# Kernel optimization log

Hardware: AMD Instinct MI355X
Metric: run time of the kernel (lower is better)

## Reference

```python
import jax, jax.numpy as jnp
import numpy as np

N_HIDDEN = 512
N_MEMORY = 128
BUDGET = 16
BATCH = 32768


def setup_inputs() -> dict:
    key = jax.random.key(0)
    ks = jax.random.split(key, 4)
    s1 = 1.0 / np.sqrt(N_HIDDEN + N_MEMORY)
    s2 = 1.0 / np.sqrt(2048)
    return {
        "x": jax.random.normal(ks[0], (BATCH, N_HIDDEN), dtype=jnp.float32),
        "W1": jax.random.normal(ks[1], (N_HIDDEN + N_MEMORY, 2048), dtype=jnp.float32) * s1,
        "b1": jnp.zeros((2048,), dtype=jnp.float32),
        "W2": jax.random.normal(ks[2], (2048, 2048), dtype=jnp.float32) * s2,
        "b2": jnp.zeros((2048,), dtype=jnp.float32),
        "W3": jax.random.normal(ks[3], (2048, N_HIDDEN + N_MEMORY + 2), dtype=jnp.float32) * s2,
        "b3": jnp.zeros((N_HIDDEN + N_MEMORY + 2,), dtype=jnp.float32),
    }


def reference(x, W1, b1, W2, b2, W3, b3):
    batch = x.shape[0]
    dtype = x.dtype

    memory = jnp.zeros((batch, N_MEMORY), dtype=dtype).at[:, 0].set(float(BUDGET))
    halted = jnp.zeros((batch,), dtype=bool)
    final_probs = jnp.zeros((batch,), dtype=dtype)
    n_iters = jnp.zeros((batch,), dtype=dtype)  # never updated in the original forward

    def mlp(inp):
        h = jax.nn.relu(inp @ W1 + b1)
        h = jax.nn.relu(h @ W2 + b2)
        return h @ W3 + b3

    def step(carry, _):
        x, mem, halted, fp = carry
        out = mlp(jnp.concatenate([x, mem], axis=-1))  # [B, 2+H+M]
        probs = out[:, 0]
        halt_val = out[:, 1]
        hidden_out = out[:, 2:2 + N_HIDDEN]
        mem_out = out[:, 2 + N_HIDDEN:]
        active = ~halted
        # torch compacts with boolean masks; masked-where is the dense equivalent
        x = jnp.where(active[:, None], hidden_out, x)
        mem = jnp.where(active[:, None], mem_out, mem)
        halt = jax.nn.sigmoid(halt_val) > 0.5  # sigmoid().round().bool()
        newly = active & halt
        fp = jnp.where(newly, probs, fp)
        halted = halted | newly
        return (x, mem, halted, fp), None

    (x, memory, halted, final_probs), _ = jax.lax.scan(
        step, (x, memory, halted, final_probs), None, length=BUDGET)

    return jax.nn.sigmoid(final_probs), n_iters
```

## Files before the change

kernel.cpp:

```cpp
#include <hip/hip_runtime.h>
#include <math.h>

typedef _Float16 f16;
typedef _Float16 f16x8 __attribute__((ext_vector_type(8)));
typedef float f32x4 __attribute__((ext_vector_type(4)));

#define NB 32768
#define NH 512
#define NM 128
#define NIN 640
#define NHID 2048
#define NOUT 642
#define NOUTP 768
#define ITERS 16
#define S1 2048.0f
#define EPS1 4.8828125e-4f

__device__ __forceinline__ void gload16(const void* g, void* lds) {
  __builtin_amdgcn_global_load_lds(
      reinterpret_cast<const __attribute__((address_space(1))) unsigned int*>((uintptr_t)g),
      reinterpret_cast<__attribute__((address_space(3))) unsigned int*>((unsigned int)(uintptr_t)lds),
      16, 0, 0);
}

__device__ __forceinline__ f32x4 mfma16(f16x8 a, f16x8 b, f32x4 c) {
  return __builtin_amdgcn_mfma_f32_16x16x32_f16(a, b, c, 0, 0, 0);
}

__device__ __forceinline__ void split2(float v, f16& a0, f16& a1) {
  a0 = (f16)v;
  a1 = (f16)((v - (float)a0) * S1);
}

__global__ void k_prepW(const float* __restrict__ W, f16* __restrict__ WT,
                        int K, int Nreal) {
  __shared__ float tile[32][33];
  int k0 = blockIdx.x * 32, n0 = blockIdx.y * 32;
  int tx = threadIdx.x & 31, ty = threadIdx.x >> 5;
#pragma unroll
  for (int r = 0; r < 4; ++r) {
    int kk = ty + 8 * r;
    int n = n0 + tx;
    tile[kk][tx] = (n < Nreal) ? W[(size_t)(k0 + kk) * Nreal + n] : 0.0f;
  }
  __syncthreads();
#pragma unroll
  for (int r = 0; r < 4; ++r) {
    int nl = ty + 8 * r;
    float v = tile[tx][nl];
    f16 a0, a1; split2(v, a0, a1);
    size_t o = (size_t)(n0 + nl) * (2 * K) + k0 + tx;
    WT[o] = a0; WT[o + K] = a1;
  }
}

__global__ void k_splitX(const float* __restrict__ x, f16* __restrict__ xm2) {
  int i = blockIdx.x * 256 + threadIdx.x;
  int row = i >> 9, c = i & 511;
  f16 a0, a1; split2(x[i], a0, a1);
  size_t o = (size_t)row * (2 * NIN) + c;
  xm2[o] = a0; xm2[o + NIN] = a1;
}

__global__ void k_init(f16* __restrict__ xm2, float* __restrict__ fpb,
                       int* __restrict__ list0, int* __restrict__ cnt) {
  int gid = blockIdx.x * blockDim.x + threadIdx.x;
  if (gid < NB * NM) {
    int row = gid >> 7, c = gid & 127;
    size_t o = (size_t)row * (2 * NIN) + 512 + c;
    xm2[o] = (f16)((c == 0) ? 16.0f : 0.0f);
    xm2[o + NIN] = (f16)0.0f;
  }
  if (gid < NB) { fpb[gid] = 0.0f; list0[gid] = gid; }
  if (gid < 32) cnt[gid] = (gid == 0) ? NB : 0;
}


#define GEMM_PREAMBLE()                                                     \
  int tid = threadIdx.x;                                                    \
  int w = tid >> 6, lane = tid & 63;                                        \
  int lm = lane & 15, kb = lane >> 4;                                       \
  int kidx = ((kb ^ ((lm >> 1) & 3)) << 3);                                 \
  int ksrc = (((tid & 3) ^ ((tid >> 3) & 3)) << 3);                         \
  int stg = tid * 8;                                                        \
  int afo[4], bfo[2];                                                       \
  _Pragma("unroll") for (int m = 0; m < 4; ++m)                             \
    afo[m] = (m * 16 + lm) * 32 + kidx;                                     \
  _Pragma("unroll") for (int n = 0; n < 2; ++n)                             \
    bfo[n] = (w * 32 + n * 16 + lm) * 32 + kidx + 4096;                     \
  f32x4 acc0[4][2], acc1[4][2];                                             \
  _Pragma("unroll") for (int m = 0; m < 4; ++m)                             \
  _Pragma("unroll") for (int n = 0; n < 2; ++n) {                           \
    acc0[m][n] = (f32x4)0.0f; acc1[m][n] = (f32x4)0.0f;                     \
  }

#define GEMM_COMPUTE(BASE)                                                  \
  {                                                                         \
    const f16* _sb = (BASE);                                                \
    f16x8 fa0[4], fa1[4], fb0[2], fb1[2];                                   \
    _Pragma("unroll") for (int m = 0; m < 4; ++m) {                         \
      fa0[m] = *(const f16x8*)&_sb[afo[m]];                                 \
      fa1[m] = *(const f16x8*)&_sb[2048 + afo[m]];                          \
    }                                                                       \
    _Pragma("unroll") for (int n = 0; n < 2; ++n) {                         \
      fb0[n] = *(const f16x8*)&_sb[bfo[n]];                                 \
      fb1[n] = *(const f16x8*)&_sb[4096 + bfo[n]];                          \
    }                                                                       \
    __builtin_amdgcn_s_setprio(1);                                          \
    _Pragma("unroll") for (int m = 0; m < 4; ++m)                           \
    _Pragma("unroll") for (int n = 0; n < 2; ++n) {                         \
      acc0[m][n] = mfma16(fa0[m], fb0[n], acc0[m][n]);                      \
      acc1[m][n] = mfma16(fa0[m], fb1[n], acc1[m][n]);                      \
      acc1[m][n] = mfma16(fa1[m], fb0[n], acc1[m][n]);                      \
    }                                                                       \
    __builtin_amdgcn_s_setprio(0);                                          \
  }

#define STAGE6(K0, DST, PSA, PSB)                                           \
  {                                                                         \
    _Pragma("unroll") for (int s = 0; s < 2; ++s)                           \
      gload16(pA + s * (PSA) + (K0), (DST) + s * 2048 + stg);               \
    _Pragma("unroll") for (int s = 0; s < 2; ++s) {                         \
      gload16(pB + s * (PSB) + (K0), (DST) + 4096 + s * 4096 + stg);        \
      gload16(pB2 + s * (PSB) + (K0), (DST) + 6144 + s * 4096 + stg);       \
    }                                                                       \
  }

#define GEMM_PIPELOOP(KTOT, PSA, PSB)                                       \
  STAGE6(0, &SB[0], PSA, PSB);                                              \
  __syncthreads();                                                          \
  {                                                                         \
    int pb = 0;                                                             \
    for (int k0 = 0; k0 < (KTOT); k0 += 32, pb ^= 1) {                      \
      if (k0 + 32 < (KTOT))                                                 \
        STAGE6(k0 + 32, pb ? &SB[0] : &SB[12288], PSA, PSB);                \
      GEMM_COMPUTE(pb ? &SB[12288] : &SB[0]);                               \
      __syncthreads();                                                      \
    }                                                                       \
  }

#define COMBINE(m, n, q) (acc0[m][n][q] + EPS1 * acc1[m][n][q])

#define MAP16(ID, BX, NY) int NY = ((ID) & 7) + 8 * (((ID) >> 3) & 1); int BX = (ID) >> 4;

__global__ __launch_bounds__(256) void k_l1(
    const f16* __restrict__ xm2, const f16* __restrict__ WT,
    const float* __restrict__ b1, f16* __restrict__ h1,
    const int* __restrict__ list, const int* __restrict__ cntp,
    int chunk_off, int chunk_rows) {
  int cnt = *cntp;
  MAP16(blockIdx.x, bx, ny);
  int lm0 = bx * 64;
  if (chunk_off + lm0 >= cnt) return;
  int lim = cnt - chunk_off; if (lim > chunk_rows) lim = chunk_rows;
  int n0 = ny * 128;

  __shared__ f16 SB[2 * 12288];
  GEMM_PREAMBLE();

  int pu = chunk_off + lm0 + (tid >> 2);
  int idx = list[pu < cnt ? pu : (cnt - 1)];
  const f16* pA = xm2 + (size_t)idx * (2 * NIN) + ksrc;
  const f16* pB = WT + (size_t)(n0 + (tid >> 2)) * (2 * NIN) + ksrc;
  const f16* pB2 = pB + (size_t)64 * (2 * NIN);

  GEMM_PIPELOOP(NIN, NIN, NIN);

#pragma unroll
  for (int n = 0; n < 2; ++n) {
    int col = n0 + w * 32 + n * 16 + lm;
    float bb = b1[col];
#pragma unroll
    for (int m = 0; m < 4; ++m) {
#pragma unroll
      for (int q = 0; q < 4; ++q) {
        int gr = lm0 + m * 16 + kb * 4 + q;
        if (gr < lim) {
          float v = fmaxf(COMBINE(m, n, q) + bb, 0.0f);
          f16 a0, a1; split2(v, a0, a1);
          size_t o = (size_t)gr * (2 * NHID) + col;
          h1[o] = a0; h1[o + NHID] = a1;
        }
      }
    }
  }
}

__global__ __launch_bounds__(256) void k_l2(
    const f16* __restrict__ h1, const f16* __restrict__ WT,
    const float* __restrict__ b2, f16* __restrict__ h2,
    const int* __restrict__ cntp, int chunk_off, int chunk_rows) {
  int cnt = *cntp;
  MAP16(blockIdx.x, bx, ny);
  int lm0 = bx * 64;
  if (chunk_off + lm0 >= cnt) return;
  int lim = cnt - chunk_off; if (lim > chunk_rows) lim = chunk_rows;
  int n0 = ny * 128;

  __shared__ f16 SB[2 * 12288];
  GEMM_PREAMBLE();

  const f16* pA = h1 + (size_t)(lm0 + (tid >> 2)) * (2 * NHID) + ksrc;
  const f16* pB = WT + (size_t)(n0 + (tid >> 2)) * (2 * NHID) + ksrc;
  const f16* pB2 = pB + (size_t)64 * (2 * NHID);

  GEMM_PIPELOOP(NHID, NHID, NHID);

#pragma unroll
  for (int n = 0; n < 2; ++n) {
    int col = n0 + w * 32 + n * 16 + lm;
    float bb = b2[col];
#pragma unroll
    for (int m = 0; m < 4; ++m) {
#pragma unroll
      for (int q = 0; q < 4; ++q) {
        int gr = lm0 + m * 16 + kb * 4 + q;
        if (gr < lim) {
          float v = fmaxf(COMBINE(m, n, q) + bb, 0.0f);
          f16 a0, a1; split2(v, a0, a1);
          size_t o = (size_t)gr * (2 * NHID) + col;
          h2[o] = a0; h2[o + NHID] = a1;
        }
      }
    }
  }
}

__global__ __launch_bounds__(256) void k_l3(
    const f16* __restrict__ h2, const f16* __restrict__ WT,
    const float* __restrict__ b3, f16* __restrict__ xm2,
    float* __restrict__ probs, float* __restrict__ hv,
    const int* __restrict__ list, const int* __restrict__ cntp,
    int chunk_off, int chunk_rows) {
  int cnt = *cntp;
  int id = blockIdx.x;
  int bx = id / 6, ny = id - bx * 6;
  int lm0 = bx * 64;
  if (chunk_off + lm0 >= cnt) return;
  int lim = cnt - chunk_off; if (lim > chunk_rows) lim = chunk_rows;
  int n0 = ny * 128;

  __shared__ f16 SB[2 * 12288];
  GEMM_PREAMBLE();

  const f16* pA = h2 + (size_t)(lm0 + (tid >> 2)) * (2 * NHID) + ksrc;
  const f16* pB = WT + (size_t)(n0 + (tid >> 2)) * (2 * NHID) + ksrc;
  const f16* pB2 = pB + (size_t)64 * (2 * NHID);

  GEMM_PIPELOOP(NHID, NHID, NHID);

  float bb[2]; int colv[2];
#pragma unroll
  for (int n = 0; n < 2; ++n) {
    colv[n] = n0 + w * 32 + n * 16 + lm;
    bb[n] = (colv[n] < NOUT) ? b3[colv[n]] : 0.0f;
  }
#pragma unroll
  for (int m = 0; m < 4; ++m) {
#pragma unroll
    for (int q = 0; q < 4; ++q) {
      int gr = lm0 + m * 16 + kb * 4 + q;
      if (gr >= lim) continue;
      int r = list[chunk_off + gr];
#pragma unroll
      for (int n = 0; n < 2; ++n) {
        int col = colv[n];
        if (col >= NOUT) continue;
        float v = COMBINE(m, n, q) + bb[n];
        if (col == 0) {
          probs[r] = v;
        } else if (col == 1) {
          hv[r] = v;
        } else if (col < 2 + NH) {
          f16 a0, a1; split2(v, a0, a1);
          size_t o = (size_t)r * (2 * NIN) + (col - 2);
          xm2[o] = a0; xm2[o + NIN] = a1;
        } else {
          f16 a0, a1; split2(v, a0, a1);
          size_t o = (size_t)r * (2 * NIN) + 512 + (col - 2 - NH);
          xm2[o] = a0; xm2[o + NIN] = a1;
        }
      }
    }
  }
}

__global__ void k_update(const int* __restrict__ listc, int* __restrict__ listn,
                         const float* __restrict__ hv, const float* __restrict__ probs,
                         float* __restrict__ fpb, const int* __restrict__ cntc,
                         int* __restrict__ cntn) {
  int i = blockIdx.x * blockDim.x + threadIdx.x;
  if (i >= *cntc) return;
  int r = listc[i];
  if (hv[r] > 0.0f) {
    fpb[r] = probs[r];
  } else {
    int pos = atomicAdd(cntn, 1);
    listn[pos] = r;
  }
}

__global__ void k_final(const float* __restrict__ fpb, float* __restrict__ out) {
  int i = blockIdx.x * blockDim.x + threadIdx.x;
  if (i < NB) {
    out[i] = 1.0f / (1.0f + expf(-fpb[i]));
    out[NB + i] = 0.0f;
  }
}

extern "C" void kernel_launch(void* const* d_in, const int* in_sizes, int n_in,
                              void* d_out, int out_size, void* d_ws, size_t ws_size,
                              hipStream_t stream) {
  const float* x  = (const float*)d_in[0];
  const float* W1 = (const float*)d_in[1];
  const float* b1 = (const float*)d_in[2];
  const float* W2 = (const float*)d_in[3];
  const float* b2 = (const float*)d_in[4];
  const float* W3 = (const float*)d_in[5];
  const float* b3 = (const float*)d_in[6];
  float* out = (float*)d_out;

  char* p = (char*)d_ws;
  auto alloc = [&](size_t bytes) {
    char* r = p;
    p += (bytes + 255) & ~(size_t)255;
    return r;
  };
  f16* xm2  = (f16*)alloc((size_t)NB * 2 * NIN * 2);
  f16* W1T  = (f16*)alloc((size_t)NHID * 2 * NIN * 2);
  f16* W2T  = (f16*)alloc((size_t)NHID * 2 * NHID * 2);
  f16* W3T  = (f16*)alloc((size_t)NOUTP * 2 * NHID * 2);
  float* probs = (float*)alloc((size_t)NB * 4);
  float* hvb   = (float*)alloc((size_t)NB * 4);
  float* fpb   = (float*)alloc((size_t)NB * 4);
  int* list0   = (int*)alloc((size_t)NB * 4);
  int* list1   = (int*)alloc((size_t)NB * 4);
  int* cnt     = (int*)alloc(32 * 4);

  size_t used = (size_t)(p - (char*)d_ws);
  size_t remain = (ws_size > used) ? (ws_size - used) : 0;
  long long chl = (long long)(remain / ((size_t)2 * 2 * NHID * 2));
  int CH = (int)(chl > NB ? NB : chl);
  CH &= ~127;
  if (CH < 128) CH = 128;
  f16* h1 = (f16*)alloc((size_t)CH * 2 * NHID * 2);
  f16* h2 = (f16*)alloc((size_t)CH * 2 * NHID * 2);
  int nchunks = (NB + CH - 1) / CH;

  k_prepW<<<dim3(NIN / 32, NHID / 32), 256, 0, stream>>>(W1, W1T, NIN, NHID);
  k_prepW<<<dim3(NHID / 32, NHID / 32), 256, 0, stream>>>(W2, W2T, NHID, NHID);
  k_prepW<<<dim3(NHID / 32, NOUTP / 32), 256, 0, stream>>>(W3, W3T, NHID, NOUT);
  k_splitX<<<(NB * NH) / 256, 256, 0, stream>>>(x, xm2);
  k_init<<<(NB * NM) / 256, 256, 0, stream>>>(xm2, fpb, list0, cnt);

  for (int t = 0; t < ITERS; ++t) {
    const int* lc = (t & 1) ? list1 : list0;
    int* ln       = (t & 1) ? list0 : list1;
    const int* cc = cnt + t;
    int* cn       = cnt + t + 1;
    for (int c = 0; c < nchunks; ++c) {
      int off = c * CH;
      int rows = NB - off; if (rows > CH) rows = CH;
      int g1 = (CH / 64) * 16;
      k_l1<<<g1, 256, 0, stream>>>(xm2, W1T, b1, h1, lc, cc, off, rows);
      k_l2<<<g1, 256, 0, stream>>>(h1, W2T, b2, h2, cc, off, rows);
      int g3 = (CH / 64) * 6;
      k_l3<<<g3, 256, 0, stream>>>(h2, W3T, b3, xm2, probs, hvb, lc, cc, off, rows);
    }
    k_update<<<NB / 256, 256, 0, stream>>>(lc, ln, hvb, probs, fpb, cc, cn);
  }
  k_final<<<NB / 256, 256, 0, stream>>>(fpb, out);
}
```

Before: 4.392 ms.

## Enlarge GEMM block tile to 128x128 with 2x2 wave layout

Each GEMM block now covers 128 rows by 128 columns instead of 64x128. The four waves are arranged 2x2, each computing a 64x64 subtile with 4x4 MFMA accumulators. The goal is more reuse of each LDS fragment per MFMA and less global and LDS traffic per flop. In exchange, registers double (acc0/acc1 now 4x4) and LDS per block grows to 64KB, with launch_bounds(256,2) added to keep two blocks per CU. Grids are halved, and tail chunks with few active rows waste more work per block.

```diff
diff --git a/kernel.cpp b/kernel.cpp
--- a/kernel.cpp
+++ b/kernel.cpp
@@ -79,36 +79,37 @@
 #define GEMM_PREAMBLE()                                                     \
   int tid = threadIdx.x;                                                    \
   int w = tid >> 6, lane = tid & 63;                                        \
+  int wr = w >> 1, wc = w & 1;                                              \
   int lm = lane & 15, kb = lane >> 4;                                       \
   int kidx = ((kb ^ ((lm >> 1) & 3)) << 3);                                 \
   int ksrc = (((tid & 3) ^ ((tid >> 3) & 3)) << 3);                         \
   int stg = tid * 8;                                                        \
-  int afo[4], bfo[2];                                                       \
+  int afo[4], bfo[4];                                                       \
   _Pragma("unroll") for (int m = 0; m < 4; ++m)                             \
-    afo[m] = (m * 16 + lm) * 32 + kidx;                                     \
-  _Pragma("unroll") for (int n = 0; n < 2; ++n)                             \
-    bfo[n] = (w * 32 + n * 16 + lm) * 32 + kidx + 4096;                     \
-  f32x4 acc0[4][2], acc1[4][2];                                             \
+    afo[m] = (wr * 64 + m * 16 + lm) * 32 + kidx;                           \
+  _Pragma("unroll") for (int n = 0; n < 4; ++n)                             \
+    bfo[n] = (wc * 64 + n * 16 + lm) * 32 + kidx + 8192;                    \
+  f32x4 acc0[4][4], acc1[4][4];                                             \
   _Pragma("unroll") for (int m = 0; m < 4; ++m)                             \
-  _Pragma("unroll") for (int n = 0; n < 2; ++n) {                           \
+  _Pragma("unroll") for (int n = 0; n < 4; ++n) {                           \
     acc0[m][n] = (f32x4)0.0f; acc1[m][n] = (f32x4)0.0f;                     \
   }
 
 #define GEMM_COMPUTE(BASE)                                                  \
   {                                                                         \
     const f16* _sb = (BASE);                                                \
-    f16x8 fa0[4], fa1[4], fb0[2], fb1[2];                                   \
+    f16x8 fa0[4], fa1[4], fb0[4], fb1[4];                                   \
     _Pragma("unroll") for (int m = 0; m < 4; ++m) {                         \
       fa0[m] = *(const f16x8*)&_sb[afo[m]];                                 \
-      fa1[m] = *(const f16x8*)&_sb[2048 + afo[m]];                          \
-    }                                                                       \
-    _Pragma("unroll") for (int n = 0; n < 2; ++n) {                         \
+      fa1[m] = *(const f16x8*)&_sb[4096 + afo[m]];                          \
+    }                                                                       \
+    _Pragma("unroll") for (int n = 0; n < 4; ++n) {                         \
       fb0[n] = *(const f16x8*)&_sb[bfo[n]];                                 \
       fb1[n] = *(const f16x8*)&_sb[4096 + bfo[n]];                          \
     }                                                                       \
     __builtin_amdgcn_s_setprio(1);                                          \
     _Pragma("unroll") for (int m = 0; m < 4; ++m)                           \
-    _Pragma("unroll") for (int n = 0; n < 2; ++n) {                         \
+    _Pragma("unroll") for (int n = 0; n < 4; ++n) {                         \
       acc0[m][n] = mfma16(fa0[m], fb0[n], acc0[m][n]);                      \
       acc1[m][n] = mfma16(fa0[m], fb1[n], acc1[m][n]);                      \
       acc1[m][n] = mfma16(fa1[m], fb0[n], acc1[m][n]);                      \
@@ -116,25 +117,27 @@
     __builtin_amdgcn_s_setprio(0);                                          \
   }
 
-#define STAGE6(K0, DST, PSA, PSB)                                           \
+#define STAGE8(K0, DST, PSA, PSB)                                           \
   {                                                                         \
-    _Pragma("unroll") for (int s = 0; s < 2; ++s)                           \
-      gload16(pA + s * (PSA) + (K0), (DST) + s * 2048 + stg);               \
     _Pragma("unroll") for (int s = 0; s < 2; ++s) {                         \
-      gload16(pB + s * (PSB) + (K0), (DST) + 4096 + s * 4096 + stg);        \
-      gload16(pB2 + s * (PSB) + (K0), (DST) + 6144 + s * 4096 + stg);       \
+      gload16(pA + s * (PSA) + (K0), (DST) + s * 4096 + stg);               \
+      gload16(pA2 + s * (PSA) + (K0), (DST) + 2048 + s * 4096 + stg);       \
+    }                                                                       \
+    _Pragma("unroll") for (int s = 0; s < 2; ++s) {                         \
+      gload16(pB + s * (PSB) + (K0), (DST) + 8192 + s * 4096 + stg);        \
+      gload16(pB2 + s * (PSB) + (K0), (DST) + 10240 + s * 4096 + stg);      \
     }                                                                       \
   }
 
 #define GEMM_PIPELOOP(KTOT, PSA, PSB)                                       \
-  STAGE6(0, &SB[0], PSA, PSB);                                              \
+  STAGE8(0, &SB[0], PSA, PSB);                                              \
   __syncthreads();                                                          \
   {                                                                         \
     int pb = 0;                                                             \
     for (int k0 = 0; k0 < (KTOT); k0 += 32, pb ^= 1) {                      \
       if (k0 + 32 < (KTOT))                                                 \
-        STAGE6(k0 + 32, pb ? &SB[0] : &SB[12288], PSA, PSB);                \
-      GEMM_COMPUTE(pb ? &SB[12288] : &SB[0]);                               \
+        STAGE8(k0 + 32, pb ? &SB[0] : &SB[16384], PSA, PSB);                \
+      GEMM_COMPUTE(pb ? &SB[16384] : &SB[0]);                               \
       __syncthreads();                                                      \
     }                                                                       \
   }
@@ -143,38 +146,41 @@
 
 #define MAP16(ID, BX, NY) int NY = ((ID) & 7) + 8 * (((ID) >> 3) & 1); int BX = (ID) >> 4;
 
-__global__ __launch_bounds__(256) void k_l1(
+__global__ __launch_bounds__(256, 2) void k_l1(
     const f16* __restrict__ xm2, const f16* __restrict__ WT,
     const float* __restrict__ b1, f16* __restrict__ h1,
     const int* __restrict__ list, const int* __restrict__ cntp,
     int chunk_off, int chunk_rows) {
   int cnt = *cntp;
   MAP16(blockIdx.x, bx, ny);
-  int lm0 = bx * 64;
+  int lm0 = bx * 128;
   if (chunk_off + lm0 >= cnt) return;
   int lim = cnt - chunk_off; if (lim > chunk_rows) lim = chunk_rows;
   int n0 = ny * 128;
 
-  __shared__ f16 SB[2 * 12288];
+  __shared__ f16 SB[2 * 16384];
   GEMM_PREAMBLE();
 
   int pu = chunk_off + lm0 + (tid >> 2);
+  int pu2 = pu + 64;
   int idx = list[pu < cnt ? pu : (cnt - 1)];
+  int idx2 = list[pu2 < cnt ? pu2 : (cnt - 1)];
   const f16* pA = xm2 + (size_t)idx * (2 * NIN) + ksrc;
+  const f16* pA2 = xm2 + (size_t)idx2 * (2 * NIN) + ksrc;
   const f16* pB = WT + (size_t)(n0 + (tid >> 2)) * (2 * NIN) + ksrc;
   const f16* pB2 = pB + (size_t)64 * (2 * NIN);
 
   GEMM_PIPELOOP(NIN, NIN, NIN);
 
 #pragma unroll
-  for (int n = 0; n < 2; ++n) {
-    int col = n0 + w * 32 + n * 16 + lm;
+  for (int n = 0; n < 4; ++n) {
+    int col = n0 + wc * 64 + n * 16 + lm;
     float bb = b1[col];
 #pragma unroll
     for (int m = 0; m < 4; ++m) {
 #pragma unroll
       for (int q = 0; q < 4; ++q) {
-        int gr = lm0 + m * 16 + kb * 4 + q;
+        int gr = lm0 + wr * 64 + m * 16 + kb * 4 + q;
         if (gr < lim) {
           float v = fmaxf(COMBINE(m, n, q) + bb, 0.0f);
           f16 a0, a1; split2(v, a0, a1);
@@ -186,35 +192,36 @@
   }
 }
 
-__global__ __launch_bounds__(256) void k_l2(
+__global__ __launch_bounds__(256, 2) void k_l2(
     const f16* __restrict__ h1, const f16* __restrict__ WT,
     const float* __restrict__ b2, f16* __restrict__ h2,
     const int* __restrict__ cntp, int chunk_off, int chunk_rows) {
   int cnt = *cntp;
   MAP16(blockIdx.x, bx, ny);
-  int lm0 = bx * 64;
+  int lm0 = bx * 128;
   if (chunk_off + lm0 >= cnt) return;
   int lim = cnt - chunk_off; if (lim > chunk_rows) lim = chunk_rows;
   int n0 = ny * 128;
 
-  __shared__ f16 SB[2 * 12288];
+  __shared__ f16 SB[2 * 16384];
   GEMM_PREAMBLE();
 
   const f16* pA = h1 + (size_t)(lm0 + (tid >> 2)) * (2 * NHID) + ksrc;
+  const f16* pA2 = pA + (size_t)64 * (2 * NHID);
   const f16* pB = WT + (size_t)(n0 + (tid >> 2)) * (2 * NHID) + ksrc;
   const f16* pB2 = pB + (size_t)64 * (2 * NHID);
 
   GEMM_PIPELOOP(NHID, NHID, NHID);
 
 #pragma unroll
-  for (int n = 0; n < 2; ++n) {
-    int col = n0 + w * 32 + n * 16 + lm;
+  for (int n = 0; n < 4; ++n) {
+    int col = n0 + wc * 64 + n * 16 + lm;
     float bb = b2[col];
 #pragma unroll
     for (int m = 0; m < 4; ++m) {
 #pragma unroll
       for (int q = 0; q < 4; ++q) {
-        int gr = lm0 + m * 16 + kb * 4 + q;
+        int gr = lm0 + wr * 64 + m * 16 + kb * 4 + q;
         if (gr < lim) {
           float v = fmaxf(COMBINE(m, n, q) + bb, 0.0f);
           f16 a0, a1; split2(v, a0, a1);
@@ -226,7 +233,7 @@
   }
 }
 
-__global__ __launch_bounds__(256) void k_l3(
+__global__ __launch_bounds__(256, 2) void k_l3(
     const f16* __restrict__ h2, const f16* __restrict__ WT,
     const float* __restrict__ b3, f16* __restrict__ xm2,
     float* __restrict__ probs, float* __restrict__ hv,
@@ -235,35 +242,36 @@
   int cnt = *cntp;
   int id = blockIdx.x;
   int bx = id / 6, ny = id - bx * 6;
-  int lm0 = bx * 64;
+  int lm0 = bx * 128;
   if (chunk_off + lm0 >= cnt) return;
   int lim = cnt - chunk_off; if (lim > chunk_rows) lim = chunk_rows;
   int n0 = ny * 128;
 
-  __shared__ f16 SB[2 * 12288];
+  __shared__ f16 SB[2 * 16384];
   GEMM_PREAMBLE();
 
   const f16* pA = h2 + (size_t)(lm0 + (tid >> 2)) * (2 * NHID) + ksrc;
+  const f16* pA2 = pA + (size_t)64 * (2 * NHID);
   const f16* pB = WT + (size_t)(n0 + (tid >> 2)) * (2 * NHID) + ksrc;
   const f16* pB2 = pB + (size_t)64 * (2 * NHID);
 
   GEMM_PIPELOOP(NHID, NHID, NHID);
 
-  float bb[2]; int colv[2];
-#pragma unroll
-  for (int n = 0; n < 2; ++n) {
-    colv[n] = n0 + w * 32 + n * 16 + lm;
+  float bb[4]; int colv[4];
+#pragma unroll
+  for (int n = 0; n < 4; ++n) {
+    colv[n] = n0 + wc * 64 + n * 16 + lm;
     bb[n] = (colv[n] < NOUT) ? b3[colv[n]] : 0.0f;
   }
 #pragma unroll
   for (int m = 0; m < 4; ++m) {
 #pragma unroll
     for (int q = 0; q < 4; ++q) {
-      int gr = lm0 + m * 16 + kb * 4 + q;
+      int gr = lm0 + wr * 64 + m * 16 + kb * 4 + q;
       if (gr >= lim) continue;
       int r = list[chunk_off + gr];
 #pragma unroll
-      for (int n = 0; n < 2; ++n) {
+      for (int n = 0; n < 4; ++n) {
         int col = colv[n];
         if (col >= NOUT) continue;
         float v = COMBINE(m, n, q) + bb[n];
@@ -361,10 +369,10 @@
     for (int c = 0; c < nchunks; ++c) {
       int off = c * CH;
       int rows = NB - off; if (rows > CH) rows = CH;
-      int g1 = (CH / 64) * 16;
+      int g1 = (CH / 128) * 16;
       k_l1<<<g1, 256, 0, stream>>>(xm2, W1T, b1, h1, lc, cc, off, rows);
       k_l2<<<g1, 256, 0, stream>>>(h1, W2T, b2, h2, cc, off, rows);
-      int g3 = (CH / 64) * 6;
+      int g3 = (CH / 128) * 6;
       k_l3<<<g3, 256, 0, stream>>>(h2, W3T, b3, xm2, probs, hvb, lc, cc, off, rows);
     }
     k_update<<<NB / 256, 256, 0, stream>>>(lc, ln, hvb, probs, fpb, cc, cn);
```

After: 3.993 ms. -9.1%, faster.
